# Kernel tuning notes

Hardware: AMD Instinct MI355X
Metric: run time of the kernel (lower is better)

Reference implementation:

```python
import jax, jax.numpy as jnp
import numpy as np

N_NODES = 200000
N_GRAPHS = 4000


def _sage_conv(x, src, dst, W_l, b_l, W_r, num_nodes):
    # PyG SAGEConv (aggr='mean'): out = lin_l(mean_{j in N(i)} x_j) + lin_r(x_i)
    msg_sum = jax.ops.segment_sum(x[src], dst, num_segments=num_nodes)      # [N, d]
    deg = jax.ops.segment_sum(jnp.ones_like(src, dtype=x.dtype), dst,
                              num_segments=num_nodes)                       # [N]
    mean_nbr = msg_sum / jnp.maximum(deg, 1.0)[:, None]
    return mean_nbr @ W_l.T + b_l + x @ W_r.T


def setup_inputs() -> dict:
    key = jax.random.key(0)
    ks = jax.random.split(key, 10)
    in_ch, hid, out = 32, 64, 2
    E = 3200000
    x = jax.random.normal(ks[0], (N_NODES, in_ch), dtype=jnp.float32)
    edge_index = jax.random.randint(ks[1], (2, E), 0, N_NODES, dtype=jnp.int64)
    batch = jnp.sort(jax.random.randint(ks[2], (N_NODES,), 0, N_GRAPHS, dtype=jnp.int64))

    def glorot(k, shape):
        lim = 1.0 / np.sqrt(shape[1])
        return jax.random.uniform(k, shape, jnp.float32, -lim, lim)

    return {
        "x": x,
        "edge_index": edge_index,
        "batch": batch,
        "W1_l": glorot(ks[3], (hid, in_ch)),
        "b1": jnp.zeros((hid,), jnp.float32),
        "W1_r": glorot(ks[4], (hid, in_ch)),
        "W2_l": glorot(ks[5], (hid, hid)),
        "b2": jnp.zeros((hid,), jnp.float32),
        "W2_r": glorot(ks[6], (hid, hid)),
        "W_lin": glorot(ks[7], (out, hid)),
        "b_lin": jnp.zeros((out,), jnp.float32),
    }


def reference(x, edge_index, batch, W1_l, b1, W1_r, W2_l, b2, W2_r, W_lin, b_lin):
    src, dst = edge_index[0], edge_index[1]
    h = jax.nn.relu(_sage_conv(x, src, dst, W1_l, b1, W1_r, N_NODES))
    h = jax.nn.relu(_sage_conv(h, src, dst, W2_l, b2, W2_r, N_NODES))
    # global_mean_pool over graph ids
    pool_sum = jax.ops.segment_sum(h, batch, num_segments=N_GRAPHS)          # [G, 64]
    cnt = jax.ops.segment_sum(jnp.ones_like(batch, dtype=h.dtype), batch,
                              num_segments=N_GRAPHS)                          # [G]
    pooled = pool_sum / jnp.maximum(cnt, 1.0)[:, None]
    return pooled @ W_lin.T + b_lin
```

## Files before the change

kernel.cpp:

```cpp
#include <hip/hip_runtime.h>
#include <hip/hip_bf16.h>


#define WS_ALIGN 64
#define EPB 4096
#define BSHIFT 8
#define BNODES 256
#define BCAP 6144
#define MAXNB 1024

typedef short bf16x8 __attribute__((ext_vector_type(8)));
typedef float f32x4 __attribute__((ext_vector_type(4)));

__device__ inline unsigned short f2bf(float f) {
    unsigned u = __float_as_uint(f);
    return (unsigned short)((u + 0x7fffu + ((u >> 16) & 1u)) >> 16);
}

__device__ inline void acc8(const uint4 u, float* a) {
    a[0] += __uint_as_float(u.x << 16);
    a[1] += __uint_as_float(u.x & 0xffff0000u);
    a[2] += __uint_as_float(u.y << 16);
    a[3] += __uint_as_float(u.y & 0xffff0000u);
    a[4] += __uint_as_float(u.z << 16);
    a[5] += __uint_as_float(u.z & 0xffff0000u);
    a[6] += __uint_as_float(u.w << 16);
    a[7] += __uint_as_float(u.w & 0xffff0000u);
}


__global__ void prep_kernel(const float* __restrict__ x, unsigned short* __restrict__ xb,
                            const float* __restrict__ W1_l, const float* __restrict__ W1_r,
                            const float* __restrict__ W2_l, const float* __restrict__ W2_r,
                            unsigned short* __restrict__ whi1, unsigned short* __restrict__ whi2,
                            int* __restrict__ bucketCursor, float* __restrict__ pool,
                            int N, int NB, int G, int total4) {
    const int gid = blockIdx.x * blockDim.x + threadIdx.x;
    if (gid < total4) {
        const float4 v = reinterpret_cast<const float4*>(x)[gid];
        ushort4 o;
        o.x = f2bf(v.x); o.y = f2bf(v.y); o.z = f2bf(v.z); o.w = f2bf(v.w);
        reinterpret_cast<ushort4*>(xb)[gid] = o;
    }
    if (gid < NB) bucketCursor[gid] = gid * BCAP;
    if (gid < G * 64) pool[gid] = 0.0f;
    if (gid < 64 * 64) {
        const int o = gid >> 6, k = gid & 63;
        const float v = (k < 32) ? W1_l[o * 32 + k] : W1_r[o * 32 + (k - 32)];
        whi1[gid] = f2bf(v);
    }
    if (gid < 64 * 128) {
        const int o = gid >> 7, k = gid & 127;
        const float v = (k < 64) ? W2_l[o * 64 + k] : W2_r[o * 64 + (k - 64)];
        whi2[gid] = f2bf(v);
    }
}


__global__ __launch_bounds__(256) void bucket_scatter_kernel(const int* __restrict__ src,
                                                             const int* __restrict__ dst,
                                                             int* __restrict__ bucketCursor,
                                                             unsigned* __restrict__ bucketData,
                                                             int E, int NB) {
    __shared__ int hist[MAXNB];
    __shared__ int cur[MAXNB];
    const int t = threadIdx.x;
    for (int i = t; i < MAXNB; i += 256) hist[i] = 0;
    __syncthreads();
    const int eBase = blockIdx.x * EPB + t;
    int s[16], b[16], dl[16];
#pragma unroll
    for (int j = 0; j < 16; ++j) {
        int e = eBase + j * 256;
        if (e < E) {
            int d = dst[e];
            s[j]  = src[e];
            b[j]  = d >> BSHIFT;
            dl[j] = d & (BNODES - 1);
            atomicAdd(&hist[b[j]], 1);
        } else {
            b[j] = -1;
        }
    }
    __syncthreads();
    for (int bb = t; bb < NB; bb += 256)
        if (hist[bb] > 0) cur[bb] = atomicAdd(&bucketCursor[bb], hist[bb]);
    __syncthreads();
#pragma unroll
    for (int j = 0; j < 16; ++j) {
        if (b[j] >= 0) {
            int pos = atomicAdd(&cur[b[j]], 1);
            if (pos < (b[j] + 1) * BCAP)
                bucketData[pos] = ((unsigned)s[j] << BSHIFT) | (unsigned)dl[j];
        }
    }
}

__global__ __launch_bounds__(256) void csr_build_kernel(const unsigned* __restrict__ bucketData,
                                                        const int* __restrict__ bucketCursor,
                                                        int* __restrict__ offs,
                                                        int* __restrict__ offe,
                                                        int* __restrict__ csr_src,
                                                        int N) {
    __shared__ int cnt[BNODES];
    __shared__ int sscan[BNODES];
    __shared__ int cur[BNODES];
    const int t   = threadIdx.x;
    const int bkt = blockIdx.x;
    const int nodeBase = bkt << BSHIFT;
    const int regionBase = bkt * BCAP;
    const int count = min(bucketCursor[bkt] - regionBase, BCAP);
    cnt[t] = 0;
    __syncthreads();
    for (int k = regionBase + t; k < regionBase + count; k += 256)
        atomicAdd(&cnt[bucketData[k] & (BNODES - 1)], 1);
    __syncthreads();
    int v0 = cnt[t];
    sscan[t] = v0;
    __syncthreads();
    for (int off = 1; off < 256; off <<= 1) {
        int v = (t >= off) ? sscan[t - off] : 0;
        __syncthreads();
        sscan[t] += v;
        __syncthreads();
    }
    const int excl = sscan[t] - v0;
    cur[t] = excl;
    const int node = nodeBase + t;
    if (node < N) {
        offs[node] = regionBase + excl;
        offe[node] = regionBase + excl + v0;
    }
    __syncthreads();
    for (int k = regionBase + t; k < regionBase + count; k += 256) {
        const unsigned v = bucketData[k];
        const int d = (int)(v & (BNODES - 1));
        const int pos = regionBase + atomicAdd(&cur[d], 1);
        csr_src[pos] = (int)(v >> BSHIFT);
    }
}


template <int D>
__global__ void agg_bf16_kernel(const unsigned short* __restrict__ featb,
                                const int* __restrict__ csr_src,
                                const int* __restrict__ offs,
                                const int* __restrict__ offe,
                                unsigned short* __restrict__ aggb, int N) {
    constexpr int TPN = D / 8;
    int tid  = blockIdx.x * blockDim.x + threadIdx.x;
    int node = tid / TPN;
    int part = tid % TPN;
    if (node >= N) return;
    const int beg = offs[node];
    const int end = offe[node];
    const uint4* base = reinterpret_cast<const uint4*>(featb);
    float a[8] = {0.f, 0.f, 0.f, 0.f, 0.f, 0.f, 0.f, 0.f};
    int k = beg;
    for (; k + 8 <= end; k += 8) {
        int s[8];
#pragma unroll
        for (int j = 0; j < 8; ++j) s[j] = csr_src[k + j];
        uint4 u[8];
#pragma unroll
        for (int j = 0; j < 8; ++j) u[j] = base[(size_t)s[j] * TPN + part];
#pragma unroll
        for (int j = 0; j < 8; ++j) acc8(u[j], a);
    }
    for (; k + 4 <= end; k += 4) {
        const int s0 = csr_src[k + 0];
        const int s1 = csr_src[k + 1];
        const int s2 = csr_src[k + 2];
        const int s3 = csr_src[k + 3];
        const uint4 u0 = base[(size_t)s0 * TPN + part];
        const uint4 u1 = base[(size_t)s1 * TPN + part];
        const uint4 u2 = base[(size_t)s2 * TPN + part];
        const uint4 u3 = base[(size_t)s3 * TPN + part];
        acc8(u0, a); acc8(u1, a); acc8(u2, a); acc8(u3, a);
    }
    for (; k < end; ++k) {
        const uint4 u = base[(size_t)csr_src[k] * TPN + part];
        acc8(u, a);
    }
    const float inv = 1.0f / fmaxf((float)(end - beg), 1.0f);
    ushort4 lo, hi;
    lo.x = f2bf(a[0] * inv); lo.y = f2bf(a[1] * inv);
    lo.z = f2bf(a[2] * inv); lo.w = f2bf(a[3] * inv);
    hi.x = f2bf(a[4] * inv); hi.y = f2bf(a[5] * inv);
    hi.z = f2bf(a[6] * inv); hi.w = f2bf(a[7] * inv);
    unsigned short* dstp = aggb + (size_t)node * D + part * 8;
    *reinterpret_cast<ushort4*>(dstp)     = lo;
    *reinterpret_cast<ushort4*>(dstp + 4) = hi;
}


template <int DIN, bool POOL>
__launch_bounds__(256)
__global__ void mfma_dense_kernel(const unsigned short* __restrict__ aggb,
                                  const unsigned short* __restrict__ xinb,
                                  const unsigned short* __restrict__ whi,
                                  const float* __restrict__ bias,
                                  unsigned short* __restrict__ houtb,
                                  const int* __restrict__ batch,
                                  float* __restrict__ pool_sum,
                                  int N, int nSteps) {
    constexpr int K   = 2 * DIN;
    constexpr int STR = K + 8;
    constexpr int D8  = DIN / 8;
    constexpr int K8  = K / 8;
    __shared__ unsigned short A_s[64 * STR];
    __shared__ unsigned short Bh_s[64 * STR];
    const int tid = threadIdx.x;
    const int nodeBase = blockIdx.x * 64;

    for (int i = tid; i < 64 * D8 * 2; i += 256) {
        const int half = i / (64 * D8);
        const int j = i % (64 * D8);
        const int node = j / D8, q = j % D8;
        const int n = min(nodeBase + node, N - 1);
        const unsigned short* srcp = half ? xinb : aggb;
        const uint4 u = *reinterpret_cast<const uint4*>(srcp + (size_t)n * DIN + q * 8);
        *reinterpret_cast<uint4*>(&A_s[node * STR + half * DIN + q * 8]) = u;
    }
    for (int i = tid; i < 64 * K8; i += 256) {
        const int o = i / K8, q = i % K8;
        const uint4 u = *reinterpret_cast<const uint4*>(whi + (size_t)o * K + q * 8);
        *reinterpret_cast<uint4*>(&Bh_s[o * STR + q * 8]) = u;
    }
    __syncthreads();

    const int lane = tid & 63;
    const int wave = tid >> 6;
    const int lr = lane & 15;
    const int q  = lane >> 4;
    f32x4 acc[4];
#pragma unroll
    for (int t = 0; t < 4; ++t) {
        const float b = bias[t * 16 + lr];
        acc[t] = (f32x4){b, b, b, b};
    }
    const unsigned short* Arow = &A_s[(wave * 16 + lr) * STR + q * 8];
    for (int s = 0; s < nSteps; ++s) {
        const bf16x8 af = *reinterpret_cast<const bf16x8*>(Arow + s * 32);
#pragma unroll
        for (int t = 0; t < 4; ++t) {
            const bf16x8 bh = *reinterpret_cast<const bf16x8*>(
                &Bh_s[(t * 16 + lr) * STR + s * 32 + q * 8]);
            acc[t] = __builtin_amdgcn_mfma_f32_16x16x32_bf16(af, bh, acc[t], 0, 0, 0);
        }
    }

    if (POOL) {
        float ag[4] = {0.f, 0.f, 0.f, 0.f};
        int gcur = -1;
        for (int reg = 0; reg < 4; ++reg) {
            const int n = nodeBase + wave * 16 + q * 4 + reg;
            if (n >= N) break;
            const int g = batch[n];
            if (g != gcur) {
                if (gcur >= 0) {
#pragma unroll
                    for (int t = 0; t < 4; ++t)
                        atomicAdd(&pool_sum[(size_t)gcur * 64 + t * 16 + lr], ag[t]);
                }
                gcur = g;
                ag[0] = ag[1] = ag[2] = ag[3] = 0.f;
            }
#pragma unroll
            for (int t = 0; t < 4; ++t)
                ag[t] += fmaxf(acc[t][reg], 0.0f);
        }
        if (gcur >= 0) {
#pragma unroll
            for (int t = 0; t < 4; ++t)
                atomicAdd(&pool_sum[(size_t)gcur * 64 + t * 16 + lr], ag[t]);
        }
    } else {
        for (int reg = 0; reg < 4; ++reg) {
            const int n = nodeBase + wave * 16 + q * 4 + reg;
            if (n >= N) break;
#pragma unroll
            for (int t = 0; t < 4; ++t)
                houtb[(size_t)n * 64 + t * 16 + lr] = f2bf(fmaxf(acc[t][reg], 0.0f));
        }
    }
}


__device__ inline int lower_bound_batch(const int* __restrict__ batch, int N, int key) {
    int lo = 0, hi = N;
    while (lo < hi) {
        const int mid = (lo + hi) >> 1;
        if (batch[mid] < key) lo = mid + 1; else hi = mid;
    }
    return lo;
}

__global__ void final_kernel(const float* __restrict__ pool_sum,
                             const int* __restrict__ batch,
                             const float* __restrict__ W_lin,
                             const float* __restrict__ b_lin,
                             float* __restrict__ out, int G, int N) {
    int t = blockIdx.x * blockDim.x + threadIdx.x;
    if (t >= G * 2) return;
    int g = t >> 1, o = t & 1;
    const int c0 = lower_bound_batch(batch, N, g);
    const int c1 = lower_bound_batch(batch, N, g + 1);
    float inv = 1.0f / fmaxf((float)(c1 - c0), 1.0f);
    float acc = b_lin[o];
#pragma unroll
    for (int c = 0; c < 64; ++c)
        acc = fmaf(pool_sum[(size_t)g * 64 + c] * inv, W_lin[o * 64 + c], acc);
    out[t] = acc;
}

extern "C" void kernel_launch(void* const* d_in, const int* in_sizes, int n_in,
                              void* d_out, int out_size, void* d_ws, size_t ws_size,
                              hipStream_t stream) {
    const float* x     = (const float*)d_in[0];
    const int*   ei    = (const int*)d_in[1];
    const int*   batch = (const int*)d_in[2];
    const float* W1_l  = (const float*)d_in[3];
    const float* b1    = (const float*)d_in[4];
    const float* W1_r  = (const float*)d_in[5];
    const float* W2_l  = (const float*)d_in[6];
    const float* b2    = (const float*)d_in[7];
    const float* W2_r  = (const float*)d_in[8];
    const float* W_lin = (const float*)d_in[9];
    const float* b_lin = (const float*)d_in[10];

    const int N = in_sizes[0] / 32;
    const int E = in_sizes[1] / 2;
    const int G = out_size / 2;
    const int* src = ei;
    const int* dst = ei + E;
    const int NB = (N + BNODES - 1) >> BSHIFT;

    char* p = (char*)d_ws;
    auto carve = [&](size_t bytes) -> void* {
        void* r = (void*)p;
        p += (bytes + (WS_ALIGN - 1)) / WS_ALIGN * WS_ALIGN;
        return r;
    };
    int*            bucketCursor = (int*)carve((size_t)MAXNB * 4);
    unsigned*       bucketData   = (unsigned*)carve((size_t)NB * BCAP * 4);
    int*            offs         = (int*)carve((size_t)N * 4);
    int*            offe         = (int*)carve((size_t)N * 4);
    int*            csr_src      = (int*)carve((size_t)NB * BCAP * 4);
    unsigned short* xb           = (unsigned short*)carve((size_t)N * 32 * 2);
    unsigned short* aggb         = (unsigned short*)carve((size_t)N * 64 * 2);
    unsigned short* h1b          = (unsigned short*)carve((size_t)N * 64 * 2);
    unsigned short* whi1         = (unsigned short*)carve(64 * 64 * 2);
    unsigned short* whi2         = (unsigned short*)carve(64 * 128 * 2);
    float*          pool         = (float*)carve((size_t)G * 64 * 4);
    float*          out          = (float*)d_out;

    const int TB = 256;
    const int total4 = N * 32 / 4;
    prep_kernel<<<(total4 + TB - 1) / TB, TB, 0, stream>>>(
        x, xb, W1_l, W1_r, W2_l, W2_r, whi1, whi2, bucketCursor, pool,
        N, NB, G, total4);
    bucket_scatter_kernel<<<(E + EPB - 1) / EPB, TB, 0, stream>>>(src, dst, bucketCursor,
                                                                  bucketData, E, NB);
    csr_build_kernel<<<NB, TB, 0, stream>>>(bucketData, bucketCursor, offs, offe, csr_src, N);

    agg_bf16_kernel<32><<<((size_t)N * 4 + TB - 1) / TB, TB, 0, stream>>>(
        xb, csr_src, offs, offe, aggb, N);
    mfma_dense_kernel<32, false><<<(N + 63) / 64, TB, 0, stream>>>(
        aggb, xb, whi1, b1, h1b, nullptr, nullptr, N, 2);

    agg_bf16_kernel<64><<<((size_t)N * 8 + TB - 1) / TB, TB, 0, stream>>>(
        h1b, csr_src, offs, offe, aggb, N);
    mfma_dense_kernel<64, true><<<(N + 63) / 64, TB, 0, stream>>>(
        aggb, h1b, whi2, b2, nullptr, batch, pool, N, 4);

    final_kernel<<<(G * 2 + TB - 1) / TB, TB, 0, stream>>>(pool, batch, W_lin, b_lin,
                                                           out, G, N);
}
```

Measured before the change: 355.7 us.

## Fuse neighbor mean aggregation into MFMA dense kernel via shared memory

Merges the separate gather-aggregate kernel into the MFMA dense kernel. Each block of 256 threads aggregates neighbours for its 64 nodes, four threads per node, and writes the bf16 means straight into the shared A tile instead of through a global aggb buffer. This removes two kernel launches and the global write and read-back of the aggregated features. In exchange each thread handles more features for the 64-wide layer (V=2), which raises register pressure and lowers gather parallelism per node compared with the previous 8 threads per node.

Result: no change. 354.5 us (-0.3%).

```diff
diff --git a/kernel.cpp b/kernel.cpp
--- a/kernel.cpp
+++ b/kernel.cpp
@@ -141,91 +141,110 @@
 }
 
 
-template <int D>
-__global__ void agg_bf16_kernel(const unsigned short* __restrict__ featb,
-                                const int* __restrict__ csr_src,
-                                const int* __restrict__ offs,
-                                const int* __restrict__ offe,
-                                unsigned short* __restrict__ aggb, int N) {
-    constexpr int TPN = D / 8;
-    int tid  = blockIdx.x * blockDim.x + threadIdx.x;
-    int node = tid / TPN;
-    int part = tid % TPN;
-    if (node >= N) return;
-    const int beg = offs[node];
-    const int end = offe[node];
-    const uint4* base = reinterpret_cast<const uint4*>(featb);
-    float a[8] = {0.f, 0.f, 0.f, 0.f, 0.f, 0.f, 0.f, 0.f};
-    int k = beg;
-    for (; k + 8 <= end; k += 8) {
-        int s[8];
-#pragma unroll
-        for (int j = 0; j < 8; ++j) s[j] = csr_src[k + j];
-        uint4 u[8];
-#pragma unroll
-        for (int j = 0; j < 8; ++j) u[j] = base[(size_t)s[j] * TPN + part];
-#pragma unroll
-        for (int j = 0; j < 8; ++j) acc8(u[j], a);
-    }
-    for (; k + 4 <= end; k += 4) {
-        const int s0 = csr_src[k + 0];
-        const int s1 = csr_src[k + 1];
-        const int s2 = csr_src[k + 2];
-        const int s3 = csr_src[k + 3];
-        const uint4 u0 = base[(size_t)s0 * TPN + part];
-        const uint4 u1 = base[(size_t)s1 * TPN + part];
-        const uint4 u2 = base[(size_t)s2 * TPN + part];
-        const uint4 u3 = base[(size_t)s3 * TPN + part];
-        acc8(u0, a); acc8(u1, a); acc8(u2, a); acc8(u3, a);
-    }
-    for (; k < end; ++k) {
-        const uint4 u = base[(size_t)csr_src[k] * TPN + part];
-        acc8(u, a);
-    }
-    const float inv = 1.0f / fmaxf((float)(end - beg), 1.0f);
-    ushort4 lo, hi;
-    lo.x = f2bf(a[0] * inv); lo.y = f2bf(a[1] * inv);
-    lo.z = f2bf(a[2] * inv); lo.w = f2bf(a[3] * inv);
-    hi.x = f2bf(a[4] * inv); hi.y = f2bf(a[5] * inv);
-    hi.z = f2bf(a[6] * inv); hi.w = f2bf(a[7] * inv);
-    unsigned short* dstp = aggb + (size_t)node * D + part * 8;
-    *reinterpret_cast<ushort4*>(dstp)     = lo;
-    *reinterpret_cast<ushort4*>(dstp + 4) = hi;
-}
-
-
 template <int DIN, bool POOL>
 __launch_bounds__(256)
-__global__ void mfma_dense_kernel(const unsigned short* __restrict__ aggb,
-                                  const unsigned short* __restrict__ xinb,
-                                  const unsigned short* __restrict__ whi,
-                                  const float* __restrict__ bias,
-                                  unsigned short* __restrict__ houtb,
-                                  const int* __restrict__ batch,
-                                  float* __restrict__ pool_sum,
-                                  int N, int nSteps) {
+__global__ void fused_agg_mfma_kernel(const unsigned short* __restrict__ featb,
+                                      const unsigned short* __restrict__ whi,
+                                      const float* __restrict__ bias,
+                                      const int* __restrict__ csr_src,
+                                      const int* __restrict__ offs,
+                                      const int* __restrict__ offe,
+                                      unsigned short* __restrict__ houtb,
+                                      const int* __restrict__ batch,
+                                      float* __restrict__ pool_sum,
+                                      int N, int nSteps) {
     constexpr int K   = 2 * DIN;
     constexpr int STR = K + 8;
     constexpr int D8  = DIN / 8;
     constexpr int K8  = K / 8;
+    constexpr int V   = DIN / 32;
     __shared__ unsigned short A_s[64 * STR];
     __shared__ unsigned short Bh_s[64 * STR];
     const int tid = threadIdx.x;
     const int nodeBase = blockIdx.x * 64;
 
-    for (int i = tid; i < 64 * D8 * 2; i += 256) {
-        const int half = i / (64 * D8);
-        const int j = i % (64 * D8);
-        const int node = j / D8, q = j % D8;
-        const int n = min(nodeBase + node, N - 1);
-        const unsigned short* srcp = half ? xinb : aggb;
-        const uint4 u = *reinterpret_cast<const uint4*>(srcp + (size_t)n * DIN + q * 8);
-        *reinterpret_cast<uint4*>(&A_s[node * STR + half * DIN + q * 8]) = u;
-    }
     for (int i = tid; i < 64 * K8; i += 256) {
         const int o = i / K8, q = i % K8;
         const uint4 u = *reinterpret_cast<const uint4*>(whi + (size_t)o * K + q * 8);
         *reinterpret_cast<uint4*>(&Bh_s[o * STR + q * 8]) = u;
+    }
+    for (int i = tid; i < 64 * D8; i += 256) {
+        const int node = i / D8, q = i % D8;
+        const int n = min(nodeBase + node, N - 1);
+        const uint4 u = *reinterpret_cast<const uint4*>(featb + (size_t)n * DIN + q * 8);
+        *reinterpret_cast<uint4*>(&A_s[node * STR + DIN + q * 8]) = u;
+    }
+
+    {
+        const int node = tid >> 2;
+        const int part = tid & 3;
+        const int n = nodeBase + node;
+        unsigned short* dp = &A_s[node * STR + part * (8 * V)];
+        if (n < N) {
+            const int beg = offs[n];
+            const int end = offe[n];
+            const uint4* base = reinterpret_cast<const uint4*>(featb);
+            float a[8 * V];
+#pragma unroll
+            for (int i = 0; i < 8 * V; ++i) a[i] = 0.f;
+            int k = beg;
+            for (; k + 8 <= end; k += 8) {
+                int s[8];
+#pragma unroll
+                for (int j = 0; j < 8; ++j) s[j] = csr_src[k + j];
+                uint4 u[8 * V];
+#pragma unroll
+                for (int j = 0; j < 8; ++j)
+#pragma unroll
+                    for (int v = 0; v < V; ++v)
+                        u[j * V + v] = base[(size_t)s[j] * D8 + part * V + v];
+#pragma unroll
+                for (int j = 0; j < 8; ++j)
+#pragma unroll
+                    for (int v = 0; v < V; ++v)
+                        acc8(u[j * V + v], &a[v * 8]);
+            }
+            for (; k + 4 <= end; k += 4) {
+                int s[4];
+#pragma unroll
+                for (int j = 0; j < 4; ++j) s[j] = csr_src[k + j];
+                uint4 u[4 * V];
+#pragma unroll
+                for (int j = 0; j < 4; ++j)
+#pragma unroll
+                    for (int v = 0; v < V; ++v)
+                        u[j * V + v] = base[(size_t)s[j] * D8 + part * V + v];
+#pragma unroll
+                for (int j = 0; j < 4; ++j)
+#pragma unroll
+                    for (int v = 0; v < V; ++v)
+                        acc8(u[j * V + v], &a[v * 8]);
+            }
+            for (; k < end; ++k) {
+                const int s = csr_src[k];
+#pragma unroll
+                for (int v = 0; v < V; ++v) {
+                    const uint4 u = base[(size_t)s * D8 + part * V + v];
+                    acc8(u, &a[v * 8]);
+                }
+            }
+            const float inv = 1.0f / fmaxf((float)(end - beg), 1.0f);
+#pragma unroll
+            for (int v = 0; v < V; ++v) {
+                ushort4 lo, hi;
+                lo.x = f2bf(a[v * 8 + 0] * inv); lo.y = f2bf(a[v * 8 + 1] * inv);
+                lo.z = f2bf(a[v * 8 + 2] * inv); lo.w = f2bf(a[v * 8 + 3] * inv);
+                hi.x = f2bf(a[v * 8 + 4] * inv); hi.y = f2bf(a[v * 8 + 5] * inv);
+                hi.z = f2bf(a[v * 8 + 6] * inv); hi.w = f2bf(a[v * 8 + 7] * inv);
+                *reinterpret_cast<ushort4*>(dp + v * 8)     = lo;
+                *reinterpret_cast<ushort4*>(dp + v * 8 + 4) = hi;
+            }
+        } else {
+            const ushort4 z = {0, 0, 0, 0};
+#pragma unroll
+            for (int v = 0; v < 2 * V; ++v)
+                *reinterpret_cast<ushort4*>(dp + v * 4) = z;
+        }
     }
     __syncthreads();
 
@@ -348,7 +367,6 @@
     int*            offe         = (int*)carve((size_t)N * 4);
     int*            csr_src      = (int*)carve((size_t)NB * BCAP * 4);
     unsigned short* xb           = (unsigned short*)carve((size_t)N * 32 * 2);
-    unsigned short* aggb         = (unsigned short*)carve((size_t)N * 64 * 2);
     unsigned short* h1b          = (unsigned short*)carve((size_t)N * 64 * 2);
     unsigned short* whi1         = (unsigned short*)carve(64 * 64 * 2);
     unsigned short* whi2         = (unsigned short*)carve(64 * 128 * 2);
@@ -364,15 +382,11 @@
                                                                   bucketData, E, NB);
     csr_build_kernel<<<NB, TB, 0, stream>>>(bucketData, bucketCursor, offs, offe, csr_src, N);
 
-    agg_bf16_kernel<32><<<((size_t)N * 4 + TB - 1) / TB, TB, 0, stream>>>(
-        xb, csr_src, offs, offe, aggb, N);
-    mfma_dense_kernel<32, false><<<(N + 63) / 64, TB, 0, stream>>>(
-        aggb, xb, whi1, b1, h1b, nullptr, nullptr, N, 2);
-
-    agg_bf16_kernel<64><<<((size_t)N * 8 + TB - 1) / TB, TB, 0, stream>>>(
-        h1b, csr_src, offs, offe, aggb, N);
-    mfma_dense_kernel<64, true><<<(N + 63) / 64, TB, 0, stream>>>(
-        aggb, h1b, whi2, b2, nullptr, batch, pool, N, 4);
+    fused_agg_mfma_kernel<32, false><<<(N + 63) / 64, TB, 0, stream>>>(
+        xb, whi1, b1, csr_src, offs, offe, h1b, nullptr, nullptr, N, 2);
+
+    fused_agg_mfma_kernel<64, true><<<(N + 63) / 64, TB, 0, stream>>>(
+        h1b, whi2, b2, csr_src, offs, offe, nullptr, batch, pool, N, 4);
 
     final_kernel<<<(G * 2 + TB - 1) / TB, TB, 0, stream>>>(pool, batch, W_lin, b_lin,
                                                            out, G, N);
```
